# Performance work log

Hardware: AMD Instinct MI355X
Metric: run time of the kernel (lower is better)

The kernel has to match this reference:

```python
import jax, jax.numpy as jnp
import numpy as np

IN_FEATURES = 256
N_HEADS = 4
N_HIDDEN = 128  # out_features, concat=False
SLOPE = 0.1
NEG_INF = -9e15


def setup_inputs() -> dict:
    key = jax.random.key(0)
    k1, k2, k3, k4 = jax.random.split(key, 4)
    N = 8192
    h = jax.random.normal(k1, (N, IN_FEATURES), dtype=jnp.float32)
    adj_mat = jax.random.randint(k2, (N, N), 0, 2, dtype=jnp.int32)
    # xavier_normal with gain=1.414
    std_W = 1.414 * (2.0 / (IN_FEATURES + N_HIDDEN * N_HEADS)) ** 0.5
    W = jax.random.normal(k3, (IN_FEATURES, N_HIDDEN * N_HEADS), dtype=jnp.float32) * std_W
    std_a = 1.414 * (2.0 / (2 * N_HIDDEN + 1)) ** 0.5
    a = jax.random.normal(k4, (N_HEADS, 2 * N_HIDDEN, 1), dtype=jnp.float32) * std_a
    return {"h": h, "adj_mat": adj_mat, "W": W, "a": a}


def reference(h, adj_mat, W, a):
    N = h.shape[0]
    # linear projection -> [H, N, d]
    ht = (h @ W).reshape(N, N_HEADS, N_HIDDEN).transpose(1, 0, 2)
    # dropout is identity (eval / p effectively 0), then LeakyReLU
    ht = jnp.where(ht >= 0, ht, SLOPE * ht)
    # additive attention scores: src[h,i] + tgt[h,j]
    src = jnp.einsum('hnd,hd->hn', ht, a[:, :N_HIDDEN, 0])  # [H, N]
    tgt = jnp.einsum('hnd,hd->hn', ht, a[:, N_HIDDEN:, 0])  # [H, N]
    e = src[:, :, None] + tgt[:, None, :]                   # [H, N, N]
    e = jnp.where(adj_mat[None, :, :] > 0, e, NEG_INF)
    attn = jax.nn.softmax(e, axis=-1)
    # weighted sum and mean over heads (concat=False)
    out = jnp.einsum('hnm,hmd->hnd', attn, ht).mean(axis=0)  # [N, d]
    return out
```

## Files before the change

kernel.cpp:

```cpp
#include <hip/hip_runtime.h>


typedef unsigned short u16;
typedef unsigned int u32;
using bf16x8 = __attribute__((ext_vector_type(8))) short;
using f32x4  = __attribute__((ext_vector_type(4))) float;

typedef const void __attribute__((address_space(1))) gas_void;
typedef void __attribute__((address_space(3))) las_void;
#define GLD16(g, l) __builtin_amdgcn_global_load_lds((gas_void*)(g), (las_void*)(l), 16, 0, 0)

__device__ __forceinline__ u16 f2bf(float f) {
  u32 u = __float_as_uint(f);
  return (u16)((u + 0x7FFFu + ((u >> 16) & 1u)) >> 16);
}
__device__ __forceinline__ float bf2f(u16 u) {
  return __uint_as_float(((u32)u) << 16);
}

__global__ void transpose_w(const float* __restrict__ W, float* __restrict__ Wt) {
  __shared__ float tile[32][33];
  int cb = blockIdx.x * 32, kb = blockIdx.y * 32;
  int tc = threadIdx.x & 31, tr = threadIdx.x >> 5;
  for (int p = 0; p < 32; p += 8)
    tile[tr + p][tc] = W[(size_t)(kb + tr + p) * 512 + cb + tc];
  __syncthreads();
  for (int p = 0; p < 32; p += 8)
    Wt[(size_t)(cb + tr + p) * 256 + kb + tc] = tile[tc][tr + p];
}

__global__ void ht_gemm(const float* __restrict__ h, const float* __restrict__ Wt,
                        u16* __restrict__ HT) {
  __shared__ __align__(16) u16 Abuf[128 * 40];
  __shared__ __align__(16) u16 Bbuf[128 * 40];
  int tid = threadIdx.x;
  int cb = blockIdx.x, rb = blockIdx.y;
  int r0 = rb * 128, c0 = cb * 128;
  int lane = tid & 63, wv = tid >> 6;
  int wr = wv >> 1, wc = wv & 1;
  int mrow = lane & 15, q = lane >> 4;
  int ch = tid & 7, m0 = tid >> 3;

  f32x4 acc[4][4];
#pragma unroll
  for (int i = 0; i < 4; i++)
#pragma unroll
    for (int j = 0; j < 4; j++) acc[i][j] = f32x4{0.f, 0.f, 0.f, 0.f};

  for (int kt = 0; kt < 256; kt += 32) {
    __syncthreads();
#pragma unroll
    for (int mp = 0; mp < 128; mp += 32) {
      int m = m0 + mp;
      float4 v = *(const float4*)(&h[(size_t)(r0 + m) * 256 + kt + ch * 4]);
      uint2 p;
      p.x = (u32)f2bf(v.x) | ((u32)f2bf(v.y) << 16);
      p.y = (u32)f2bf(v.z) | ((u32)f2bf(v.w) << 16);
      *(uint2*)(&Abuf[m * 40 + ch * 4]) = p;
      float4 u = *(const float4*)(&Wt[(size_t)(c0 + m) * 256 + kt + ch * 4]);
      uint2 r;
      r.x = (u32)f2bf(u.x) | ((u32)f2bf(u.y) << 16);
      r.y = (u32)f2bf(u.z) | ((u32)f2bf(u.w) << 16);
      *(uint2*)(&Bbuf[m * 40 + ch * 4]) = r;
    }
    __syncthreads();
    bf16x8 af[4], bfv[4];
#pragma unroll
    for (int i = 0; i < 4; i++)
      af[i] = *(const bf16x8*)(&Abuf[(wr * 64 + i * 16 + mrow) * 40 + q * 8]);
#pragma unroll
    for (int j = 0; j < 4; j++)
      bfv[j] = *(const bf16x8*)(&Bbuf[(wc * 64 + j * 16 + mrow) * 40 + q * 8]);
#pragma unroll
    for (int i = 0; i < 4; i++)
#pragma unroll
      for (int j = 0; j < 4; j++)
        acc[i][j] = __builtin_amdgcn_mfma_f32_16x16x32_bf16(af[i], bfv[j], acc[i][j], 0, 0, 0);
  }
#pragma unroll
  for (int i = 0; i < 4; i++)
#pragma unroll
    for (int j = 0; j < 4; j++)
#pragma unroll
      for (int r = 0; r < 4; r++) {
        int gi = r0 + wr * 64 + i * 16 + q * 4 + r;
        int gc = c0 + wc * 64 + j * 16 + mrow;
        float v = acc[i][j][r];
        v = v >= 0.f ? v : 0.1f * v;
        HT[(size_t)gi * 512 + gc] = f2bf(v);
      }
}

__global__ void build_yt(const u16* __restrict__ HT, const float* __restrict__ a,
                         u16* __restrict__ Yt) {
  __shared__ u16 sht[64][528];
  __shared__ float swv[64 * 4];
  __shared__ float sa[512];
  int t = threadIdx.x;
  int j0 = blockIdx.x * 64;
  for (int i = t; i < 512; i += 256) {
    int g = i >> 7, d = i & 127;
    sa[i] = a[g * 256 + 128 + d];
  }
#pragma unroll
  for (int p = 0; p < 16; ++p) {
    int el = t + 256 * p;
    int row = el >> 6, col8 = el & 63;
    *(uint4*)(&sht[row][col8 * 8]) = *(const uint4*)(&HT[(size_t)(j0 + row) * 512 + col8 * 8]);
  }
  __syncthreads();
  {
    int jl = t >> 2, g = t & 3;
    float acc = 0.f;
#pragma unroll
    for (int d8 = 0; d8 < 16; ++d8) {
      bf16x8 v = *(const bf16x8*)(&sht[jl][g * 128 + d8 * 8]);
#pragma unroll
      for (int u = 0; u < 8; ++u)
        acc += bf2f((u16)v[u]) * sa[g * 128 + d8 * 8 + u];
    }
    swv[jl * 4 + g] = __expf(acc);
  }
  __syncthreads();
  int oj = (t & 7) * 8, oc = t >> 3;
  for (int pass = 0; pass < 17; ++pass) {
    int c = pass * 32 + oc;
    if (c >= 528) break;
    u32 pk[4] = {0u, 0u, 0u, 0u};
    if (c < 512) {
      int g = c >> 7;
#pragma unroll
      for (int u = 0; u < 4; ++u) {
        int j = oj + 2 * u;
        float v0 = bf2f(sht[j][c]) * swv[j * 4 + g];
        float v1 = bf2f(sht[j + 1][c]) * swv[(j + 1) * 4 + g];
        pk[u] = (u32)f2bf(v0) | ((u32)f2bf(v1) << 16);
      }
    } else if (c < 516) {
      int g = c - 512;
#pragma unroll
      for (int u = 0; u < 4; ++u) {
        int j = oj + 2 * u;
        float v0 = swv[j * 4 + g];
        float v1 = swv[(j + 1) * 4 + g];
        pk[u] = (u32)f2bf(v0) | ((u32)f2bf(v1) << 16);
      }
    }
    *(uint4*)(&Yt[(size_t)c * 8192 + j0 + oj]) = make_uint4(pk[0], pk[1], pk[2], pk[3]);
  }
}

__global__ __launch_bounds__(512) void adj_gemm(const int* __restrict__ adj,
                                                const u16* __restrict__ Yt,
                                                float* __restrict__ C,
                                                float* __restrict__ S) {
  __shared__ __align__(16) u16 Abuf[128 * 32];
  __shared__ __align__(16) u16 Bbuf[512 * 32];
  __shared__ __align__(16) u16 Bden[16 * 32];
  int tid = threadIdx.x;
  int rb = blockIdx.x, kh = blockIdx.y;
  int r0 = rb * 128, k0 = kh * 2048;
  int lane = tid & 63, wv = tid >> 6;
  int wr = wv >> 2, wc = wv & 3;
  int mrow = lane & 15, q = lane >> 4;
  int am = tid >> 2, ak = (tid & 3) * 8;
  int brow = lane >> 2, bq = lane & 3;
  bool do_den = (wc == 0);

  f32x4 acc[4][8];
#pragma unroll
  for (int i = 0; i < 4; i++)
#pragma unroll
    for (int j = 0; j < 8; j++) acc[i][j] = f32x4{0.f, 0.f, 0.f, 0.f};
  f32x4 accD[4];
#pragma unroll
  for (int i = 0; i < 4; i++) accD[i] = f32x4{0.f, 0.f, 0.f, 0.f};

  for (int kt = k0; kt < k0 + 2048; kt += 32) {
    __syncthreads();
    {
      const int* ap = &adj[(size_t)(r0 + am) * 8192 + kt + ak];
      int4 v0 = *(const int4*)(ap);
      int4 v1 = *(const int4*)(ap + 4);
      uint4 p;
      p.x = 16256u * ((u32)v0.x | ((u32)v0.y << 16));
      p.y = 16256u * ((u32)v0.z | ((u32)v0.w << 16));
      p.z = 16256u * ((u32)v1.x | ((u32)v1.y << 16));
      p.w = 16256u * ((u32)v1.z | ((u32)v1.w << 16));
      *(uint4*)(&Abuf[am * 32 + ak]) = p;
    }
#pragma unroll
    for (int p = 0; p < 4; ++p)
      GLD16(&Yt[(size_t)(p * 128 + wv * 16 + brow) * 8192 + kt + bq * 8],
            &Bbuf[(p * 128 + wv * 16) * 32]);
    if (wv == 0)
      GLD16(&Yt[(size_t)(512 + brow) * 8192 + kt + bq * 8], Bden);
    __syncthreads();
    bf16x8 af[4], bfv[8];
#pragma unroll
    for (int i = 0; i < 4; i++)
      af[i] = *(const bf16x8*)(&Abuf[(wr * 64 + i * 16 + mrow) * 32 + q * 8]);
#pragma unroll
    for (int j = 0; j < 8; j++)
      bfv[j] = *(const bf16x8*)(&Bbuf[(wc * 128 + j * 16 + mrow) * 32 + q * 8]);
#pragma unroll
    for (int i = 0; i < 4; i++)
#pragma unroll
      for (int j = 0; j < 8; j++)
        acc[i][j] = __builtin_amdgcn_mfma_f32_16x16x32_bf16(af[i], bfv[j], acc[i][j], 0, 0, 0);
    if (do_den) {
      bf16x8 bd = *(const bf16x8*)(&Bden[mrow * 32 + q * 8]);
#pragma unroll
      for (int i = 0; i < 4; i++)
        accD[i] = __builtin_amdgcn_mfma_f32_16x16x32_bf16(af[i], bd, accD[i], 0, 0, 0);
    }
  }
  float* Ck = C + (size_t)kh * 8192 * 512;
#pragma unroll
  for (int i = 0; i < 4; i++)
#pragma unroll
    for (int j = 0; j < 8; j++)
#pragma unroll
      for (int r = 0; r < 4; r++) {
        int gi = r0 + wr * 64 + i * 16 + q * 4 + r;
        int gc = wc * 128 + j * 16 + mrow;
        Ck[(size_t)gi * 512 + gc] = acc[i][j][r];
      }
  if (do_den && mrow < 4) {
    float* Sk = S + (size_t)kh * 4 * 8192;
#pragma unroll
    for (int i = 0; i < 4; i++)
#pragma unroll
      for (int r = 0; r < 4; r++) {
        int gi = r0 + wr * 64 + i * 16 + q * 4 + r;
        Sk[(size_t)mrow * 8192 + gi] = accD[i][r];
      }
  }
}

__global__ void finalize_gat(const float* __restrict__ C, const float* __restrict__ S,
                             float* __restrict__ out) {
  int idx = blockIdx.x * 256 + threadIdx.x;
  int i = idx >> 7, d = idx & 127;
  float s = 0.f;
#pragma unroll
  for (int g = 0; g < 4; ++g) {
    float num = 0.f, den = 0.f;
#pragma unroll
    for (int kh = 0; kh < 4; ++kh) {
      num += C[(size_t)kh * 8192 * 512 + (size_t)i * 512 + g * 128 + d];
      den += S[(size_t)kh * 4 * 8192 + (size_t)g * 8192 + i];
    }
    s += num / den;
  }
  out[idx] = 0.25f * s;
}

extern "C" void kernel_launch(void* const* d_in, const int* in_sizes, int n_in,
                              void* d_out, int out_size, void* d_ws, size_t ws_size,
                              hipStream_t stream) {
  const float* h   = (const float*)d_in[0];
  const int*   adj = (const int*)d_in[1];
  const float* W   = (const float*)d_in[2];
  const float* a   = (const float*)d_in[3];
  float* out = (float*)d_out;
  char* ws = (char*)d_ws;
  float* Wt = (float*)(ws + 0);
  u16*   HT = (u16*)(ws + 524288);
  u16*   Yt = (u16*)(ws + 8912896);
  float* C  = (float*)(ws + 17563648);
  float* S  = (float*)(ws + 84672512);

  transpose_w<<<dim3(16, 8), 256, 0, stream>>>(W, Wt);
  ht_gemm<<<dim3(4, 64), 256, 0, stream>>>(h, Wt, HT);
  build_yt<<<dim3(128), 256, 0, stream>>>(HT, a, Yt);
  adj_gemm<<<dim3(64, 4), 512, 0, stream>>>(adj, Yt, C, S);
  finalize_gat<<<dim3(4096), 256, 0, stream>>>(C, S, out);
}
```

Measured before the change: 503.4 us.

## Double-buffer adj_gemm LDS tiles with XOR swizzle and smaller row blocks

Restructures the adjacency GEMM to use double-buffered LDS for the A (adjacency as bf16) and B (Yt) tiles. Next-tile loads are issued before the current tile's MFMAs, so there is one barrier per iteration instead of two. It also applies an XOR swizzle to LDS addresses to reduce bank conflicts. Blocks shrink to 64 rows with 256 threads and two blocks per CU, doubling the grid to 128x4. Each wave now covers all 64 rows and 128 columns, which re-reads the full B tile per 64 rows and doubles total Yt traffic, while the adjacency read stays the same.

```diff
diff --git a/kernel.cpp b/kernel.cpp
--- a/kernel.cpp
+++ b/kernel.cpp
@@ -150,22 +150,24 @@
   }
 }
 
-__global__ __launch_bounds__(512) void adj_gemm(const int* __restrict__ adj,
-                                                const u16* __restrict__ Yt,
-                                                float* __restrict__ C,
-                                                float* __restrict__ S) {
-  __shared__ __align__(16) u16 Abuf[128 * 32];
-  __shared__ __align__(16) u16 Bbuf[512 * 32];
-  __shared__ __align__(16) u16 Bden[16 * 32];
+__global__ __launch_bounds__(256, 2) void adj_gemm(const int* __restrict__ adj,
+                                                   const u16* __restrict__ Yt,
+                                                   float* __restrict__ C,
+                                                   float* __restrict__ S) {
+  __shared__ __align__(16) u16 Abuf[2][64 * 32];
+  __shared__ __align__(16) u16 Bbuf[2][512 * 32];
+  __shared__ __align__(16) u16 Bden[2][16 * 32];
   int tid = threadIdx.x;
   int rb = blockIdx.x, kh = blockIdx.y;
-  int r0 = rb * 128, k0 = kh * 2048;
+  int r0 = rb * 64, k0 = kh * 2048;
   int lane = tid & 63, wv = tid >> 6;
-  int wr = wv >> 2, wc = wv & 3;
   int mrow = lane & 15, q = lane >> 4;
-  int am = tid >> 2, ak = (tid & 3) * 8;
-  int brow = lane >> 2, bq = lane & 3;
-  bool do_den = (wc == 0);
+  int qs = q ^ ((mrow >> 1) & 3);
+  int am = tid >> 2, aq = tid & 3;
+  int asw = am * 32 + ((aq ^ ((am >> 1) & 3)) * 8);
+  const int* aptr = &adj[(size_t)(r0 + am) * 8192 + k0 + aq * 8];
+  int brow = lane >> 2;
+  int bq = (lane & 3) ^ ((lane >> 3) & 3);
 
   f32x4 acc[4][8];
 #pragma unroll
@@ -176,45 +178,85 @@
 #pragma unroll
   for (int i = 0; i < 4; i++) accD[i] = f32x4{0.f, 0.f, 0.f, 0.f};
 
-  for (int kt = k0; kt < k0 + 2048; kt += 32) {
+  {
+#pragma unroll
+    for (int p = 0; p < 8; ++p)
+      GLD16(&Yt[(size_t)(wv * 128 + p * 16 + brow) * 8192 + k0 + bq * 8],
+            &Bbuf[0][(wv * 128 + p * 16) * 32]);
+    if (wv == 0)
+      GLD16(&Yt[(size_t)(512 + brow) * 8192 + k0 + bq * 8], &Bden[0][0]);
+    int4 v0 = *(const int4*)(aptr);
+    int4 v1 = *(const int4*)(aptr + 4);
+    uint4 pk;
+    pk.x = 16256u * ((u32)v0.x | ((u32)v0.y << 16));
+    pk.y = 16256u * ((u32)v0.z | ((u32)v0.w << 16));
+    pk.z = 16256u * ((u32)v1.x | ((u32)v1.y << 16));
+    pk.w = 16256u * ((u32)v1.z | ((u32)v1.w << 16));
+    *(uint4*)(&Abuf[0][asw]) = pk;
     __syncthreads();
-    {
-      const int* ap = &adj[(size_t)(r0 + am) * 8192 + kt + ak];
-      int4 v0 = *(const int4*)(ap);
-      int4 v1 = *(const int4*)(ap + 4);
-      uint4 p;
-      p.x = 16256u * ((u32)v0.x | ((u32)v0.y << 16));
-      p.y = 16256u * ((u32)v0.z | ((u32)v0.w << 16));
-      p.z = 16256u * ((u32)v1.x | ((u32)v1.y << 16));
-      p.w = 16256u * ((u32)v1.z | ((u32)v1.w << 16));
-      *(uint4*)(&Abuf[am * 32 + ak]) = p;
-    }
-#pragma unroll
-    for (int p = 0; p < 4; ++p)
-      GLD16(&Yt[(size_t)(p * 128 + wv * 16 + brow) * 8192 + kt + bq * 8],
-            &Bbuf[(p * 128 + wv * 16) * 32]);
+  }
+
+  int cur = 0;
+  for (int t = 0; t < 63; ++t) {
+    int nxt = cur ^ 1;
+    int kt = k0 + (t + 1) * 32;
+#pragma unroll
+    for (int p = 0; p < 8; ++p)
+      GLD16(&Yt[(size_t)(wv * 128 + p * 16 + brow) * 8192 + kt + bq * 8],
+            &Bbuf[nxt][(wv * 128 + p * 16) * 32]);
     if (wv == 0)
-      GLD16(&Yt[(size_t)(512 + brow) * 8192 + kt + bq * 8], Bden);
-    __syncthreads();
+      GLD16(&Yt[(size_t)(512 + brow) * 8192 + kt + bq * 8], &Bden[nxt][0]);
+    const int* ap = aptr + (size_t)(t + 1) * 32;
+    int4 v0 = *(const int4*)(ap);
+    int4 v1 = *(const int4*)(ap + 4);
     bf16x8 af[4], bfv[8];
 #pragma unroll
     for (int i = 0; i < 4; i++)
-      af[i] = *(const bf16x8*)(&Abuf[(wr * 64 + i * 16 + mrow) * 32 + q * 8]);
+      af[i] = *(const bf16x8*)(&Abuf[cur][(i * 16 + mrow) * 32 + qs * 8]);
 #pragma unroll
     for (int j = 0; j < 8; j++)
-      bfv[j] = *(const bf16x8*)(&Bbuf[(wc * 128 + j * 16 + mrow) * 32 + q * 8]);
+      bfv[j] = *(const bf16x8*)(&Bbuf[cur][(wv * 128 + j * 16 + mrow) * 32 + qs * 8]);
 #pragma unroll
     for (int i = 0; i < 4; i++)
 #pragma unroll
       for (int j = 0; j < 8; j++)
         acc[i][j] = __builtin_amdgcn_mfma_f32_16x16x32_bf16(af[i], bfv[j], acc[i][j], 0, 0, 0);
-    if (do_den) {
-      bf16x8 bd = *(const bf16x8*)(&Bden[mrow * 32 + q * 8]);
+    if (wv == 0) {
+      bf16x8 bd = *(const bf16x8*)(&Bden[cur][mrow * 32 + qs * 8]);
 #pragma unroll
       for (int i = 0; i < 4; i++)
         accD[i] = __builtin_amdgcn_mfma_f32_16x16x32_bf16(af[i], bd, accD[i], 0, 0, 0);
     }
-  }
+    uint4 pk;
+    pk.x = 16256u * ((u32)v0.x | ((u32)v0.y << 16));
+    pk.y = 16256u * ((u32)v0.z | ((u32)v0.w << 16));
+    pk.z = 16256u * ((u32)v1.x | ((u32)v1.y << 16));
+    pk.w = 16256u * ((u32)v1.z | ((u32)v1.w << 16));
+    *(uint4*)(&Abuf[nxt][asw]) = pk;
+    __syncthreads();
+    cur = nxt;
+  }
+  {
+    bf16x8 af[4], bfv[8];
+#pragma unroll
+    for (int i = 0; i < 4; i++)
+      af[i] = *(const bf16x8*)(&Abuf[cur][(i * 16 + mrow) * 32 + qs * 8]);
+#pragma unroll
+    for (int j = 0; j < 8; j++)
+      bfv[j] = *(const bf16x8*)(&Bbuf[cur][(wv * 128 + j * 16 + mrow) * 32 + qs * 8]);
+#pragma unroll
+    for (int i = 0; i < 4; i++)
+#pragma unroll
+      for (int j = 0; j < 8; j++)
+        acc[i][j] = __builtin_amdgcn_mfma_f32_16x16x32_bf16(af[i], bfv[j], acc[i][j], 0, 0, 0);
+    if (wv == 0) {
+      bf16x8 bd = *(const bf16x8*)(&Bden[cur][mrow * 32 + qs * 8]);
+#pragma unroll
+      for (int i = 0; i < 4; i++)
+        accD[i] = __builtin_amdgcn_mfma_f32_16x16x32_bf16(af[i], bd, accD[i], 0, 0, 0);
+    }
+  }
+
   float* Ck = C + (size_t)kh * 8192 * 512;
 #pragma unroll
   for (int i = 0; i < 4; i++)
@@ -222,17 +264,17 @@
     for (int j = 0; j < 8; j++)
 #pragma unroll
       for (int r = 0; r < 4; r++) {
-        int gi = r0 + wr * 64 + i * 16 + q * 4 + r;
-        int gc = wc * 128 + j * 16 + mrow;
+        int gi = r0 + i * 16 + q * 4 + r;
+        int gc = wv * 128 + j * 16 + mrow;
         Ck[(size_t)gi * 512 + gc] = acc[i][j][r];
       }
-  if (do_den && mrow < 4) {
+  if (wv == 0 && mrow < 4) {
     float* Sk = S + (size_t)kh * 4 * 8192;
 #pragma unroll
     for (int i = 0; i < 4; i++)
 #pragma unroll
       for (int r = 0; r < 4; r++) {
-        int gi = r0 + wr * 64 + i * 16 + q * 4 + r;
+        int gi = r0 + i * 16 + q * 4 + r;
         Sk[(size_t)mrow * 8192 + gi] = accD[i][r];
       }
   }
@@ -274,6 +316,6 @@
   transpose_w<<<dim3(16, 8), 256, 0, stream>>>(W, Wt);
   ht_gemm<<<dim3(4, 64), 256, 0, stream>>>(h, Wt, HT);
   build_yt<<<dim3(128), 256, 0, stream>>>(HT, a, Yt);
-  adj_gemm<<<dim3(64, 4), 512, 0, stream>>>(adj, Yt, C, S);
+  adj_gemm<<<dim3(128, 4), 256, 0, stream>>>(adj, Yt, C, S);
   finalize_gat<<<dim3(4096), 256, 0, stream>>>(C, S, out);
 }
```

Result: no change. 509.1 us (+1.1%).
